# Kernel tuning notes

Hardware: AMD Instinct MI355X
Metric: run time of the kernel (lower is better)

The kernel has to match this reference:

```python
import jax, jax.numpy as jnp
import numpy as np

N = 100000
E = 400000
G = 2000  # number of graphs in batch
IN_DIM = 32
H = 192
L = 4
EPS = 1e-5


def setup_inputs() -> dict:
    key = jax.random.key(0)
    ks = jax.random.split(key, 20)
    x = jax.random.normal(ks[0], (N, IN_DIM), jnp.float32)
    edge_src = jax.random.randint(ks[1], (E,), 0, N, jnp.int32)
    edge_dst = jax.random.randint(ks[2], (E,), 0, N, jnp.int32)
    batch = jnp.sort(jax.random.randint(ks[3], (N,), 0, G, jnp.int32))
    s_in = 1.0 / np.sqrt(IN_DIM)
    s_h = 1.0 / np.sqrt(H)
    return {
        "x": x,
        "edge_src": edge_src,
        "edge_dst": edge_dst,
        "batch": batch,
        # layer 0 (in_dim -> H); weights stored [in, out]
        "Wrel0": jax.random.uniform(ks[4], (IN_DIM, H), jnp.float32, -s_in, s_in),
        "brel0": jax.random.uniform(ks[5], (H,), jnp.float32, -s_in, s_in),
        "Wroot0": jax.random.uniform(ks[6], (IN_DIM, H), jnp.float32, -s_in, s_in),
        # layers 1..3 stacked (H -> H)
        "Wrel": jax.random.uniform(ks[7], (L - 1, H, H), jnp.float32, -s_h, s_h),
        "brel": jax.random.uniform(ks[8], (L - 1, H), jnp.float32, -s_h, s_h),
        "Wroot": jax.random.uniform(ks[9], (L - 1, H, H), jnp.float32, -s_h, s_h),
        # batchnorm affine params for all 4 layers
        "gamma": jnp.ones((L, H), jnp.float32),
        "beta": jnp.zeros((L, H), jnp.float32),
        # head MLP and output
        "Wh1": jax.random.uniform(ks[10], (H, H), jnp.float32, -s_h, s_h),
        "bh1": jax.random.uniform(ks[11], (H,), jnp.float32, -s_h, s_h),
        "Wh2": jax.random.uniform(ks[12], (H, H), jnp.float32, -s_h, s_h),
        "bh2": jax.random.uniform(ks[13], (H,), jnp.float32, -s_h, s_h),
        "Wout": jax.random.uniform(ks[14], (H, 1), jnp.float32, -s_h, s_h),
        "bout": jax.random.uniform(ks[15], (1,), jnp.float32, -s_h, s_h),
    }


def _rel_conv(x, edge_src, edge_dst, Wrel, brel, Wroot):
    # message: lin_rel(x_j); applying the linear at node level first is the
    # same math as per-edge (linear commutes with gather) and cheaper.
    h = x @ Wrel + brel                      # [N, out]
    agg = jax.ops.segment_sum(h[edge_src], edge_dst, num_segments=N)
    return agg + x @ Wroot


def _bn_relu(h, g, b):
    # BatchNorm1d in training mode: batch stats over node dim, biased var
    mu = h.mean(axis=0)
    var = jnp.var(h, axis=0)
    h = (h - mu) * jax.lax.rsqrt(var + EPS) * g + b
    return jax.nn.relu(h)


def reference(x, edge_src, edge_dst, batch, Wrel0, brel0, Wroot0,
              Wrel, brel, Wroot, gamma, beta, Wh1, bh1, Wh2, bh2, Wout, bout):
    h = _bn_relu(_rel_conv(x, edge_src, edge_dst, Wrel0, brel0, Wroot0),
                 gamma[0], beta[0])
    for i in range(L - 1):
        h = _bn_relu(_rel_conv(h, edge_src, edge_dst, Wrel[i], brel[i], Wroot[i]),
                     gamma[i + 1], beta[i + 1])
    # global mean pool over graphs
    sums = jax.ops.segment_sum(h, batch, num_segments=G)          # [G, H]
    cnt = jax.ops.segment_sum(jnp.ones((N,), h.dtype), batch, num_segments=G)
    g = sums / jnp.maximum(cnt, 1.0)[:, None]
    # head MLP (dropout is identity at eval) + output linear
    g = jax.nn.relu(g @ Wh1 + bh1) @ Wh2 + bh2
    return g @ Wout + bout                                        # [G, 1]
```

## Files before the change

kernel.cpp:

```cpp
#include <hip/hip_runtime.h>

#define HDIM 192
#define EPS 1e-5f

typedef __attribute__((ext_vector_type(8))) _Float16 half8;
typedef __attribute__((ext_vector_type(4))) float floatx4;

__device__ __forceinline__ float h2f(ushort u) {
    union { ushort u; _Float16 h; } c; c.u = u; return (float)c.h;
}
__device__ __forceinline__ ushort f2h(float x) {
    _Float16 h = (_Float16)x;
    union { _Float16 h; ushort u; } c; c.h = h; return c.u;
}
__device__ __forceinline__ uint4 pack8(const ushort* h) {
    uint4 p;
    p.x = h[0] | ((uint)h[1] << 16); p.y = h[2] | ((uint)h[3] << 16);
    p.z = h[4] | ((uint)h[5] << 16); p.w = h[6] | ((uint)h[7] << 16);
    return p;
}

__device__ __forceinline__ void gload_lds16(const ushort* g, ushort* l) {
    __builtin_amdgcn_global_load_lds(
        (const __attribute__((address_space(1))) unsigned int*)g,
        (__attribute__((address_space(3))) unsigned int*)l, 16, 0, 0);
}

#define WAITV0() asm volatile("s_waitcnt vmcnt(0)" ::: "memory")


struct PrepArgs {
    const float* src[6];
    ushort*      dst[6];
    int K[6];
    int off[7];
};

__global__ __launch_bounds__(256) void prep_all_k(PrepArgs a)
{
    int idx = blockIdx.x * 256 + threadIdx.x;
    if (idx >= a.off[6]) return;
    int i = 0;
    #pragma unroll
    for (int t = 1; t < 6; ++t) if (idx >= a.off[t]) i = t;
    int r = idx - a.off[i];
    int K = a.K[i];
    int perMat = (K >> 5) * 12 * 64;
    int mat = r / perMat;
    r -= mat * perMat;
    int lane = r & 63;
    int ct = (r >> 6) % 12;
    int kc = r / (12 * 64);
    int col = ct * 16 + (lane & 15);
    int kb  = kc * 32 + (lane >> 4) * 8;
    const float* Wm = a.src[i] + (size_t)mat * K * HDIM;
    ushort* base = a.dst[i] + (size_t)mat * K * HDIM;
    size_t o = (size_t)kc * 6144 + (size_t)(ct * 64 + lane) * 8;
    #pragma unroll
    for (int j = 0; j < 8; ++j)
        base[o + j] = f2h(Wm[(size_t)(kb + j) * HDIM + col]);
}

__global__ __launch_bounds__(256) void conv_half_k(
    const float* __restrict__ src, ushort* __restrict__ dst, int R, int C)
{
    int OC = C >> 3;
    int idx = blockIdx.x * 256 + threadIdx.x;
    if (idx >= R * OC) return;
    int r = idx / OC;
    int o = idx - r * OC;
    float4 v0 = ((const float4*)(src + (size_t)r * C + o * 8))[0];
    float4 v1 = ((const float4*)(src + (size_t)r * C + o * 8))[1];
    float v[8] = {v0.x, v0.y, v0.z, v0.w, v1.x, v1.y, v1.z, v1.w};
    ushort h[8];
    #pragma unroll
    for (int t = 0; t < 8; ++t) h[t] = f2h(v[t]);
    *(uint4*)(dst + (size_t)r * C + o * 8) = pack8(h);
}

template<bool DUAL, bool RELU, bool DEG, bool STATS, int NKC>
__global__ __launch_bounds__(256, 3) void gemm_mfma_k(
    const ushort* __restrict__ A1h, const ushort* __restrict__ W1f,
    const ushort* __restrict__ A2h, const ushort* __restrict__ W2f,
    const float* __restrict__ degf, const float* __restrict__ bias,
    ushort* __restrict__ C, float* __restrict__ pstats, int N, int K)
{
    constexpr int KR   = NKC * 32;
    constexpr int RS   = KR + 8;
    constexpr int SLAB = 64 * RS;
    constexpr int NINSTR = SLAB / 512;
    constexpr int NCH  = DUAL ? 2 * NKC : NKC;
    constexpr int SMEMU = ((DUAL ? 2 * SLAB : SLAB) > 12800)
                            ? (DUAL ? 2 * SLAB : SLAB) : 12800;

    __shared__ float sstat[2][HDIM];
    __shared__ __align__(16) ushort smem[SMEMU];
    const int tid  = threadIdx.x;
    const int wave = tid >> 6;
    const int lane = tid & 63;
    const int row0 = blockIdx.x * 64;
    const int m16 = lane & 15;
    const int g4  = lane >> 4;

    if (STATS && tid < HDIM) { sstat[0][tid] = 0.f; sstat[1][tid] = 0.f; }

    auto stage = [&](const ushort* Ab, int slabOff) {
        #pragma unroll
        for (int i = wave; i < NINSTR; i += 4) {
            int slotB = i * 1024 + lane * 16;
            int r   = slotB / (RS * 2);
            int off = slotB - r * (RS * 2);
            if (off >= KR * 2) off = KR * 2 - 16;
            int rr = row0 + r; if (rr >= N) rr = N - 1;
            gload_lds16(Ab + (size_t)rr * KR + (off >> 1),
                        smem + slabOff + i * 512);
        }
    };

    stage(A1h, 0);
    if constexpr (DUAL) stage(A2h, SLAB);
    WAITV0();
    __builtin_amdgcn_s_barrier();
    __builtin_amdgcn_sched_barrier(0);

    auto loadB = [&](int c, half8* b) {
        bool ph = DUAL && (c >= NKC);
        int kc = ph ? c - NKC : c;
        const ushort* Bp = (ph ? W2f : W1f) + (size_t)kc * 6144
                         + (size_t)(wave * 192 + lane) * 8;
        #pragma unroll
        for (int ct = 0; ct < 3; ++ct)
            b[ct] = *(const half8*)(Bp + ct * 512);
    };

    floatx4 acc[4][3];
    #pragma unroll
    for (int s = 0; s < 4; ++s)
        #pragma unroll
        for (int ct = 0; ct < 3; ++ct) acc[s][ct] = (floatx4){0.f, 0.f, 0.f, 0.f};

    half8 bA[3], bB[3];
    loadB(0, bA);
    #pragma unroll
    for (int c = 0; c < NCH; ++c) {
        if (c + 1 < NCH) loadB(c + 1, (c & 1) ? bA : bB);
        const int base = (DUAL && c >= NKC) ? SLAB : 0;
        const int kc   = (DUAL && c >= NKC) ? c - NKC : c;
        const ushort* aB = smem + base + m16 * RS + kc * 32 + g4 * 8;
        half8 a[4];
        #pragma unroll
        for (int s = 0; s < 4; ++s)
            a[s] = *(const half8*)(aB + s * 16 * RS);
        const half8* bu = (c & 1) ? bB : bA;
        #pragma unroll
        for (int ct = 0; ct < 3; ++ct)
            #pragma unroll
            for (int s = 0; s < 4; ++s)
                acc[s][ct] = __builtin_amdgcn_mfma_f32_16x16x32_f16(a[s], bu[ct], acc[s][ct], 0, 0, 0);
    }

    __syncthreads();
    #pragma unroll
    for (int ct = 0; ct < 3; ++ct) {
        int col = wave * 48 + ct * 16 + m16;
        float bv = bias ? bias[col] : 0.f;
        float lsum = 0.f, lsq = 0.f;
        #pragma unroll
        for (int s = 0; s < 4; ++s) {
            #pragma unroll
            for (int reg = 0; reg < 4; ++reg) {
                int rloc = s * 16 + g4 * 4 + reg;
                int rr = row0 + rloc;
                int rrc = rr < N ? rr : N - 1;
                float v = acc[s][ct][reg] + (DEG ? degf[rrc] * bv : bv);
                if (STATS && rr < N) { lsum += v; lsq += v * v; }
                if (RELU) v = fmaxf(v, 0.f);
                smem[rloc * 200 + col] = f2h(v);
            }
        }
        if (STATS) {
            lsum += __shfl_xor(lsum, 16); lsum += __shfl_xor(lsum, 32);
            lsq  += __shfl_xor(lsq, 16);  lsq  += __shfl_xor(lsq, 32);
            if (g4 == 0) {
                atomicAdd(&sstat[0][col], lsum);
                atomicAdd(&sstat[1][col], lsq);
            }
        }
    }
    __syncthreads();
    {
        int rowsLeft = N - row0; if (rowsLeft > 64) rowsLeft = 64;
        int lim = rowsLeft * 24;
        ushort* Cb = C + (size_t)row0 * HDIM;
        #pragma unroll
        for (int k = 0; k < 6; ++k) {
            int u = tid + k * 256;
            if (u < lim) {
                int r  = u / 24;
                int c8 = (u - r * 24) * 8;
                *(uint4*)(Cb + (size_t)u * 8) =
                    *(const uint4*)(smem + r * 200 + c8);
            }
        }
    }
    if (STATS) {
        if (tid < HDIM) {
            float* pb = pstats + (size_t)blockIdx.x * (2 * HDIM);
            pb[tid]        = sstat[0][tid];
            pb[HDIM + tid] = sstat[1][tid];
        }
    }
}

__global__ __launch_bounds__(256) void bn_reduce_k(
    const float* __restrict__ pbuf, float* __restrict__ stats, int nb)
{
    __shared__ float red[32][9];
    int t  = threadIdx.x;
    int cl = t & 7;
    int s  = t >> 3;
    int c  = blockIdx.x * 8 + cl;
    float acc = 0.f;
    int b = s;
    for (; b + 96 < nb; b += 128) {
        float a0 = pbuf[(size_t)b * 384 + c];
        float a1 = pbuf[(size_t)(b + 32) * 384 + c];
        float a2 = pbuf[(size_t)(b + 64) * 384 + c];
        float a3 = pbuf[(size_t)(b + 96) * 384 + c];
        acc += a0 + a1 + a2 + a3;
    }
    for (; b < nb; b += 32)
        acc += pbuf[(size_t)b * 384 + c];
    red[s][cl] = acc;
    __syncthreads();
    if (t < 8) {
        float a = 0.f;
        #pragma unroll
        for (int i = 0; i < 32; ++i) a += red[i][t];
        stats[blockIdx.x * 8 + t] = a;
    }
}

__global__ __launch_bounds__(256) void hist_k(
    const int* __restrict__ dst, int* __restrict__ deg, int E)
{
    int e = blockIdx.x * 256 + threadIdx.x;
    if (e < E) atomicAdd(&deg[dst[e]], 1);
}

__global__ __launch_bounds__(256) void block_sum_k(
    const int* __restrict__ deg, int* __restrict__ bsum, int N)
{
    __shared__ int s[256];
    int t = threadIdx.x;
    int n = blockIdx.x * 256 + t;
    s[t] = (n < N) ? deg[n] : 0;
    __syncthreads();
    for (int off = 128; off > 0; off >>= 1) {
        if (t < off) s[t] += s[t + off];
        __syncthreads();
    }
    if (t == 0) bsum[blockIdx.x] = s[0];
}

__global__ __launch_bounds__(512) void scan_bsum_k(int* __restrict__ bsum, int nb)
{
    __shared__ int s[512];
    int t = threadIdx.x;
    int v = (t < nb) ? bsum[t] : 0;
    s[t] = v;
    __syncthreads();
    for (int off = 1; off < 512; off <<= 1) {
        int u = (t >= off) ? s[t - off] : 0;
        __syncthreads();
        s[t] += u;
        __syncthreads();
    }
    if (t < nb) bsum[t] = s[t] - v;
}

__global__ __launch_bounds__(256) void row_ptr_k(
    const int* __restrict__ deg, const int* __restrict__ bsum,
    int* __restrict__ row_ptr, int* __restrict__ cursor,
    float* __restrict__ degf, int N, int E)
{
    __shared__ int s[256];
    int t = threadIdx.x;
    int n = blockIdx.x * 256 + t;
    int v = (n < N) ? deg[n] : 0;
    s[t] = v;
    __syncthreads();
    for (int off = 1; off < 256; off <<= 1) {
        int u = (t >= off) ? s[t - off] : 0;
        __syncthreads();
        s[t] += u;
        __syncthreads();
    }
    int ex = s[t] - v + bsum[blockIdx.x];
    if (n < N) {
        row_ptr[n] = ex;
        cursor[n]  = ex;
        degf[n]    = (float)v;
    }
    if (blockIdx.x == 0 && t == 0) row_ptr[N] = E;
}

__global__ __launch_bounds__(256) void fill_k(
    const int* __restrict__ src, const int* __restrict__ dst,
    int* __restrict__ cursor, int* __restrict__ col, int E)
{
    int e = blockIdx.x * 256 + threadIdx.x;
    if (e < E) {
        int p = atomicAdd(&cursor[dst[e]], 1);
        col[p] = src[e];
    }
}

__global__ __launch_bounds__(256) void gather_h_k(
    const ushort* __restrict__ xh, const int* __restrict__ row_ptr,
    const int* __restrict__ col, ushort* __restrict__ gh, int N, int K)
{
    int OC = K >> 3;
    int idx = blockIdx.x * 256 + threadIdx.x;
    if (idx >= N * OC) return;
    int n = idx / OC;
    int o = idx - n * OC;
    const ushort* hp = xh + o * 8;
    int j0 = row_ptr[n], j1 = row_ptr[n + 1];
    float acc[8] = {0.f,0.f,0.f,0.f,0.f,0.f,0.f,0.f};
    auto addrow = [&](uint4 hv) {
        uint hu[4] = {hv.x, hv.y, hv.z, hv.w};
        #pragma unroll
        for (int t = 0; t < 4; ++t) {
            acc[2*t]   += h2f((ushort)(hu[t] & 0xffffu));
            acc[2*t+1] += h2f((ushort)(hu[t] >> 16));
        }
    };
    int j = j0;
    for (; j + 3 < j1; j += 4) {
        int s0 = col[j], s1 = col[j+1], s2 = col[j+2], s3 = col[j+3];
        uint4 v0 = *(const uint4*)(hp + (size_t)s0 * K);
        uint4 v1 = *(const uint4*)(hp + (size_t)s1 * K);
        uint4 v2 = *(const uint4*)(hp + (size_t)s2 * K);
        uint4 v3 = *(const uint4*)(hp + (size_t)s3 * K);
        addrow(v0); addrow(v1); addrow(v2); addrow(v3);
    }
    for (; j < j1; ++j)
        addrow(*(const uint4*)(hp + (size_t)col[j] * K));
    ushort oh[8];
    #pragma unroll
    for (int t = 0; t < 8; ++t) oh[t] = f2h(acc[t]);
    *(uint4*)(gh + (size_t)n * K + o * 8) = pack8(oh);
}

__global__ __launch_bounds__(256) void gather_bn_k(
    const ushort* __restrict__ h, const float* __restrict__ stats,
    const float* __restrict__ gamma, const float* __restrict__ beta,
    float invN, const int* __restrict__ row_ptr, const int* __restrict__ col,
    ushort* __restrict__ xh, ushort* __restrict__ gh, int N)
{
    int idx = blockIdx.x * 256 + threadIdx.x;
    if (idx >= N * 24) return;
    int n = idx / 24;
    int o = idx - n * 24;
    int q = o * 8;
    float sc[8], sh[8];
    #pragma unroll
    for (int t = 0; t < 8; ++t) {
        float mu  = stats[q + t] * invN;
        float var = stats[HDIM + q + t] * invN - mu * mu;
        float s = gamma[q + t] * rsqrtf(var + EPS);
        sc[t] = s; sh[t] = beta[q + t] - mu * s;
    }
    const ushort* hp = h + q;
    {
        uint4 hv = *(const uint4*)(hp + (size_t)n * HDIM);
        uint hu[4] = {hv.x, hv.y, hv.z, hv.w};
        ushort oh[8];
        #pragma unroll
        for (int t = 0; t < 4; ++t) {
            float v0 = h2f((ushort)(hu[t] & 0xffffu));
            float v1 = h2f((ushort)(hu[t] >> 16));
            oh[2*t]   = f2h(fmaxf(v0 * sc[2*t]   + sh[2*t],   0.f));
            oh[2*t+1] = f2h(fmaxf(v1 * sc[2*t+1] + sh[2*t+1], 0.f));
        }
        *(uint4*)(xh + (size_t)n * HDIM + q) = pack8(oh);
    }
    int j0 = row_ptr[n], j1 = row_ptr[n + 1];
    float acc[8] = {0.f,0.f,0.f,0.f,0.f,0.f,0.f,0.f};
    auto addrow = [&](uint4 hv) {
        uint hu[4] = {hv.x, hv.y, hv.z, hv.w};
        #pragma unroll
        for (int t = 0; t < 4; ++t) {
            float v0 = h2f((ushort)(hu[t] & 0xffffu));
            float v1 = h2f((ushort)(hu[t] >> 16));
            acc[2*t]   += fmaxf(v0 * sc[2*t]   + sh[2*t],   0.f);
            acc[2*t+1] += fmaxf(v1 * sc[2*t+1] + sh[2*t+1], 0.f);
        }
    };
    int j = j0;
    for (; j + 3 < j1; j += 4) {
        int s0 = col[j], s1 = col[j+1], s2 = col[j+2], s3 = col[j+3];
        uint4 v0 = *(const uint4*)(hp + (size_t)s0 * HDIM);
        uint4 v1 = *(const uint4*)(hp + (size_t)s1 * HDIM);
        uint4 v2 = *(const uint4*)(hp + (size_t)s2 * HDIM);
        uint4 v3 = *(const uint4*)(hp + (size_t)s3 * HDIM);
        addrow(v0); addrow(v1); addrow(v2); addrow(v3);
    }
    for (; j < j1; ++j)
        addrow(*(const uint4*)(hp + (size_t)col[j] * HDIM));
    ushort oh[8];
    #pragma unroll
    for (int t = 0; t < 8; ++t) oh[t] = f2h(acc[t]);
    *(uint4*)(gh + (size_t)n * HDIM + q) = pack8(oh);
}

__global__ __launch_bounds__(192) void pool_bn_k(
    const ushort* __restrict__ h, const float* __restrict__ stats,
    const float* __restrict__ gamma, const float* __restrict__ beta,
    float invN, const int* __restrict__ batch,
    ushort* __restrict__ gsh, int G, int N)
{
    __shared__ int bounds[2];
    int g = blockIdx.x;
    int c = threadIdx.x;
    if (c < 2) {
        int key = g + c;
        int lo = 0, hi = N;
        while (lo < hi) {
            int mid = (lo + hi) >> 1;
            if (batch[mid] < key) lo = mid + 1; else hi = mid;
        }
        bounds[c] = lo;
    }
    __syncthreads();
    int r0 = bounds[0], r1 = bounds[1];
    float mu  = stats[c] * invN;
    float var = stats[HDIM + c] * invN - mu * mu;
    float sc  = gamma[c] * rsqrtf(var + EPS);
    float sh  = beta[c] - mu * sc;
    const ushort* base = h + c;
    float s = 0.f;
    for (int r = r0; r < r1; ++r)
        s += fmaxf(h2f(base[(size_t)r * HDIM]) * sc + sh, 0.f);
    float m = s / fmaxf((float)(r1 - r0), 1.f);
    gsh[(size_t)g * HDIM + c] = f2h(m);
}

__global__ __launch_bounds__(64) void out_dot_k(
    const ushort* __restrict__ g2h, const float* __restrict__ Wout,
    const float* __restrict__ bout, float* __restrict__ out, int G)
{
    int gi = blockIdx.x;
    int t = threadIdx.x;
    float s = 0.f;
    #pragma unroll
    for (int j = 0; j < 3; ++j) {
        int c = t + j * 64;
        s += h2f(g2h[(size_t)gi * HDIM + c]) * Wout[c];
    }
    #pragma unroll
    for (int off = 32; off > 0; off >>= 1) s += __shfl_down(s, off, 64);
    if (t == 0) out[gi] = s + bout[0];
}

extern "C" void kernel_launch(void* const* d_in, const int* in_sizes, int n_in,
                              void* d_out, int out_size, void* d_ws, size_t ws_size,
                              hipStream_t stream)
{
    const float* x      = (const float*)d_in[0];
    const int*   esrc   = (const int*)d_in[1];
    const int*   edst   = (const int*)d_in[2];
    const int*   batch  = (const int*)d_in[3];
    const float* Wrel0  = (const float*)d_in[4];
    const float* brel0  = (const float*)d_in[5];
    const float* Wroot0 = (const float*)d_in[6];
    const float* Wrel   = (const float*)d_in[7];
    const float* brel   = (const float*)d_in[8];
    const float* Wroot  = (const float*)d_in[9];
    const float* gamma  = (const float*)d_in[10];
    const float* beta   = (const float*)d_in[11];
    const float* Wh1    = (const float*)d_in[12];
    const float* bh1    = (const float*)d_in[13];
    const float* Wh2    = (const float*)d_in[14];
    const float* bh2    = (const float*)d_in[15];
    const float* Wout   = (const float*)d_in[16];
    const float* bout   = (const float*)d_in[17];
    float* out = (float*)d_out;

    const int N  = in_sizes[3];
    const int E  = in_sizes[1];
    const int K0 = in_sizes[0] / N;
    const int G  = out_size;
    const int nBlocks = (N + 255) / 256;
    const float invN = 1.0f / (float)N;

    char* p = (char*)d_ws;
    auto carve = [&](size_t bytes) -> void* {
        void* r = (void*)p; p += (bytes + 255) & ~(size_t)255; return r;
    };
    ushort* bufa_h= (ushort*)carve((size_t)N * HDIM * 2);
    ushort* xh    = (ushort*)carve((size_t)N * HDIM * 2);
    ushort* gh    = (ushort*)carve((size_t)N * HDIM * 2);
    ushort* gsh   = (ushort*)carve((size_t)G * HDIM * 2);
    ushort* g1h   = (ushort*)carve((size_t)G * HDIM * 2);
    ushort* g2h   = (ushort*)carve((size_t)G * HDIM * 2);
    int*    deg   = (int*)   carve((size_t)N * 4);
    float*  bnsums= (float*) carve(4 * 2 * HDIM * 4);
    size_t  zspan = (char*)(bnsums + 4 * 2 * HDIM) - (char*)deg;
    float*  degf  = (float*) carve((size_t)N * 4);
    int*    row_ptr=(int*)   carve((size_t)(N + 1) * 4);
    int*    cursor= (int*)   carve((size_t)N * 4);
    int*    col   = (int*)   carve((size_t)E * 4);
    int*    bsum  = (int*)   carve((size_t)nBlocks * 4);
    ushort* Wrel0f= (ushort*)carve((size_t)K0 * HDIM * 2);
    ushort* Wroot0f=(ushort*)carve((size_t)K0 * HDIM * 2);
    ushort* Wrelf = (ushort*)carve((size_t)3 * HDIM * HDIM * 2);
    ushort* Wrootf= (ushort*)carve((size_t)3 * HDIM * HDIM * 2);
    ushort* Wh1f  = (ushort*)carve((size_t)HDIM * HDIM * 2);
    ushort* Wh2f  = (ushort*)carve((size_t)HDIM * HDIM * 2);

    dim3 b256(256);
    const int eBlocks = (E + 255) / 256;
    const int gemmN = (N + 63) / 64;
    const int gemmG = (G + 63) / 64;

    float*  pbuf  = (float*) carve((size_t)gemmN * 2 * HDIM * 4);

    {
        PrepArgs a;
        int t0 = (K0 >> 5) * 12 * 64;
        int t1 = (HDIM >> 5) * 12 * 64;
        a.src[0] = Wrel0;  a.dst[0] = Wrel0f;  a.K[0] = K0;
        a.src[1] = Wroot0; a.dst[1] = Wroot0f; a.K[1] = K0;
        a.src[2] = Wrel;   a.dst[2] = Wrelf;   a.K[2] = HDIM;
        a.src[3] = Wroot;  a.dst[3] = Wrootf;  a.K[3] = HDIM;
        a.src[4] = Wh1;    a.dst[4] = Wh1f;    a.K[4] = HDIM;
        a.src[5] = Wh2;    a.dst[5] = Wh2f;    a.K[5] = HDIM;
        a.off[0] = 0;
        a.off[1] = a.off[0] + t0;
        a.off[2] = a.off[1] + t0;
        a.off[3] = a.off[2] + 3 * t1;
        a.off[4] = a.off[3] + 3 * t1;
        a.off[5] = a.off[4] + t1;
        a.off[6] = a.off[5] + t1;
        prep_all_k<<<(a.off[6] + 255) / 256, b256, 0, stream>>>(a);
    }
    conv_half_k<<<((N * (K0 >> 3)) + 255) / 256, b256, 0, stream>>>(x, xh, N, K0);

    hipMemsetAsync(deg, 0, zspan, stream);
    hist_k<<<eBlocks, b256, 0, stream>>>(edst, deg, E);
    block_sum_k<<<nBlocks, b256, 0, stream>>>(deg, bsum, N);
    scan_bsum_k<<<1, dim3(512), 0, stream>>>(bsum, nBlocks);
    row_ptr_k<<<nBlocks, b256, 0, stream>>>(deg, bsum, row_ptr, cursor, degf, N, E);
    fill_k<<<eBlocks, b256, 0, stream>>>(esrc, edst, cursor, col, E);

    gather_h_k<<<((N * (K0 >> 3)) + 255) / 256, b256, 0, stream>>>(
        xh, row_ptr, col, gh, N, K0);
    gemm_mfma_k<true, false, true, true, 1><<<gemmN, b256, 0, stream>>>(
        gh, Wrel0f, xh, Wroot0f, degf, brel0, bufa_h, pbuf, N, K0);
    bn_reduce_k<<<48, b256, 0, stream>>>(pbuf, bnsums, gemmN);

    for (int l = 1; l < 4; ++l) {
        const ushort* Wrf = Wrelf  + (size_t)(l - 1) * HDIM * HDIM;
        const ushort* Wtf = Wrootf + (size_t)(l - 1) * HDIM * HDIM;
        const float*  br  = brel   + (size_t)(l - 1) * HDIM;
        gather_bn_k<<<(N * 24 + 255) / 256, b256, 0, stream>>>(
            bufa_h, bnsums + (l - 1) * 2 * HDIM,
            gamma + (l - 1) * HDIM, beta + (l - 1) * HDIM, invN,
            row_ptr, col, xh, gh, N);
        gemm_mfma_k<true, false, true, true, 6><<<gemmN, b256, 0, stream>>>(
            gh, Wrf, xh, Wtf, degf, br, bufa_h, pbuf, N, HDIM);
        bn_reduce_k<<<48, b256, 0, stream>>>(pbuf, bnsums + l * 2 * HDIM, gemmN);
    }

    pool_bn_k<<<G, dim3(192), 0, stream>>>(
        bufa_h, bnsums + 3 * 2 * HDIM, gamma + 3 * HDIM, beta + 3 * HDIM,
        invN, batch, gsh, G, N);

    gemm_mfma_k<false, true, false, false, 6><<<gemmG, b256, 0, stream>>>(
        gsh, Wh1f, nullptr, nullptr, nullptr, bh1, g1h, nullptr, G, HDIM);
    gemm_mfma_k<false, false, false, false, 6><<<gemmG, b256, 0, stream>>>(
        g1h, Wh2f, nullptr, nullptr, nullptr, bh2, g2h, nullptr, G, HDIM);
    out_dot_k<<<G, dim3(64), 0, stream>>>(g2h, Wout, bout, out, G);
}
```

Baseline: 474.1 us.

## Fuse BatchNorm+ReLU of the root operand into the GEMM LDS stage

The gather kernel no longer writes a normalized copy (xh) of the previous layer's activations. Instead, the dual GEMM stages the raw previous-layer half activations into LDS and applies BatchNorm scale/shift plus ReLU in place in shared memory before the MFMA loop. This removes one full N×192 half-precision write per layer and its later re-read. In exchange it adds an LDS pass and extra barriers inside the GEMM, and the GEMM now reads and writes the same buffer in place, relying on each block owning its rows.

After: 456.1 us. -3.8%, faster.

```diff
diff --git a/kernel.cpp b/kernel.cpp
--- a/kernel.cpp
+++ b/kernel.cpp
@@ -78,11 +78,13 @@
     *(uint4*)(dst + (size_t)r * C + o * 8) = pack8(h);
 }
 
-template<bool DUAL, bool RELU, bool DEG, bool STATS, int NKC>
+template<bool DUAL, bool RELU, bool DEG, bool STATS, bool BNIN, int NKC>
 __global__ __launch_bounds__(256, 3) void gemm_mfma_k(
     const ushort* __restrict__ A1h, const ushort* __restrict__ W1f,
     const ushort* __restrict__ A2h, const ushort* __restrict__ W2f,
     const float* __restrict__ degf, const float* __restrict__ bias,
+    const float* __restrict__ instats, const float* __restrict__ gammaL,
+    const float* __restrict__ betaL, float invN,
     ushort* __restrict__ C, float* __restrict__ pstats, int N, int K)
 {
     constexpr int KR   = NKC * 32;
@@ -102,7 +104,7 @@
     const int m16 = lane & 15;
     const int g4  = lane >> 4;
 
-    if (STATS && tid < HDIM) { sstat[0][tid] = 0.f; sstat[1][tid] = 0.f; }
+    if (STATS && !BNIN && tid < HDIM) { sstat[0][tid] = 0.f; sstat[1][tid] = 0.f; }
 
     auto stage = [&](const ushort* Ab, int slabOff) {
         #pragma unroll
@@ -122,6 +124,38 @@
     WAITV0();
     __builtin_amdgcn_s_barrier();
     __builtin_amdgcn_sched_barrier(0);
+
+    if constexpr (BNIN) {
+        if (tid < HDIM) {
+            float mu  = instats[tid] * invN;
+            float var = instats[HDIM + tid] * invN - mu * mu;
+            float s = gammaL[tid] * rsqrtf(var + EPS);
+            sstat[0][tid] = s;
+            sstat[1][tid] = betaL[tid] - mu * s;
+        }
+        __syncthreads();
+        {
+            int r = tid >> 2, q = tid & 3;
+            ushort* rowp = smem + SLAB + r * RS + q * 48;
+            #pragma unroll
+            for (int k = 0; k < 6; ++k) {
+                uint4 hv = *(uint4*)(rowp + k * 8);
+                uint hu[4] = {hv.x, hv.y, hv.z, hv.w};
+                ushort oh[8];
+                #pragma unroll
+                for (int e = 0; e < 4; ++e) {
+                    int ch = q * 48 + k * 8 + e * 2;
+                    float v0 = h2f((ushort)(hu[e] & 0xffffu)) * sstat[0][ch]     + sstat[1][ch];
+                    float v1 = h2f((ushort)(hu[e] >> 16))     * sstat[0][ch + 1] + sstat[1][ch + 1];
+                    oh[2*e]   = f2h(fmaxf(v0, 0.f));
+                    oh[2*e+1] = f2h(fmaxf(v1, 0.f));
+                }
+                *(uint4*)(rowp + k * 8) = pack8(oh);
+            }
+        }
+        __syncthreads();
+        if (STATS && tid < HDIM) { sstat[0][tid] = 0.f; sstat[1][tid] = 0.f; }
+    }
 
     auto loadB = [&](int c, half8* b) {
         bool ph = DUAL && (c >= NKC);
@@ -357,7 +391,7 @@
     const ushort* __restrict__ h, const float* __restrict__ stats,
     const float* __restrict__ gamma, const float* __restrict__ beta,
     float invN, const int* __restrict__ row_ptr, const int* __restrict__ col,
-    ushort* __restrict__ xh, ushort* __restrict__ gh, int N)
+    ushort* __restrict__ gh, int N)
 {
     int idx = blockIdx.x * 256 + threadIdx.x;
     if (idx >= N * 24) return;
@@ -373,19 +407,6 @@
         sc[t] = s; sh[t] = beta[q + t] - mu * s;
     }
     const ushort* hp = h + q;
-    {
-        uint4 hv = *(const uint4*)(hp + (size_t)n * HDIM);
-        uint hu[4] = {hv.x, hv.y, hv.z, hv.w};
-        ushort oh[8];
-        #pragma unroll
-        for (int t = 0; t < 4; ++t) {
-            float v0 = h2f((ushort)(hu[t] & 0xffffu));
-            float v1 = h2f((ushort)(hu[t] >> 16));
-            oh[2*t]   = f2h(fmaxf(v0 * sc[2*t]   + sh[2*t],   0.f));
-            oh[2*t+1] = f2h(fmaxf(v1 * sc[2*t+1] + sh[2*t+1], 0.f));
-        }
-        *(uint4*)(xh + (size_t)n * HDIM + q) = pack8(oh);
-    }
     int j0 = row_ptr[n], j1 = row_ptr[n + 1];
     float acc[8] = {0.f,0.f,0.f,0.f,0.f,0.f,0.f,0.f};
     auto addrow = [&](uint4 hv) {
@@ -557,20 +578,23 @@
 
     gather_h_k<<<((N * (K0 >> 3)) + 255) / 256, b256, 0, stream>>>(
         xh, row_ptr, col, gh, N, K0);
-    gemm_mfma_k<true, false, true, true, 1><<<gemmN, b256, 0, stream>>>(
-        gh, Wrel0f, xh, Wroot0f, degf, brel0, bufa_h, pbuf, N, K0);
+    gemm_mfma_k<true, false, true, true, false, 1><<<gemmN, b256, 0, stream>>>(
+        gh, Wrel0f, xh, Wroot0f, degf, brel0,
+        nullptr, nullptr, nullptr, 0.f, bufa_h, pbuf, N, K0);
     bn_reduce_k<<<48, b256, 0, stream>>>(pbuf, bnsums, gemmN);
 
     for (int l = 1; l < 4; ++l) {
         const ushort* Wrf = Wrelf  + (size_t)(l - 1) * HDIM * HDIM;
         const ushort* Wtf = Wrootf + (size_t)(l - 1) * HDIM * HDIM;
         const float*  br  = brel   + (size_t)(l - 1) * HDIM;
+        const float*  st  = bnsums + (size_t)(l - 1) * 2 * HDIM;
+        const float*  gm  = gamma  + (size_t)(l - 1) * HDIM;
+        const float*  bt  = beta   + (size_t)(l - 1) * HDIM;
         gather_bn_k<<<(N * 24 + 255) / 256, b256, 0, stream>>>(
-            bufa_h, bnsums + (l - 1) * 2 * HDIM,
-            gamma + (l - 1) * HDIM, beta + (l - 1) * HDIM, invN,
-            row_ptr, col, xh, gh, N);
-        gemm_mfma_k<true, false, true, true, 6><<<gemmN, b256, 0, stream>>>(
-            gh, Wrf, xh, Wtf, degf, br, bufa_h, pbuf, N, HDIM);
+            bufa_h, st, gm, bt, invN, row_ptr, col, gh, N);
+        gemm_mfma_k<true, false, true, true, true, 6><<<gemmN, b256, 0, stream>>>(
+            gh, Wrf, bufa_h, Wtf, degf, br,
+            st, gm, bt, invN, bufa_h, pbuf, N, HDIM);
         bn_reduce_k<<<48, b256, 0, stream>>>(pbuf, bnsums + l * 2 * HDIM, gemmN);
     }
 
@@ -578,9 +602,11 @@
         bufa_h, bnsums + 3 * 2 * HDIM, gamma + 3 * HDIM, beta + 3 * HDIM,
         invN, batch, gsh, G, N);
 
-    gemm_mfma_k<false, true, false, false, 6><<<gemmG, b256, 0, stream>>>(
-        gsh, Wh1f, nullptr, nullptr, nullptr, bh1, g1h, nullptr, G, HDIM);
-    gemm_mfma_k<false, false, false, false, 6><<<gemmG, b256, 0, stream>>>(
-        g1h, Wh2f, nullptr, nullptr, nullptr, bh2, g2h, nullptr, G, HDIM);
+    gemm_mfma_k<false, true, false, false, false, 6><<<gemmG, b256, 0, stream>>>(
+        gsh, Wh1f, nullptr, nullptr, nullptr, bh1,
+        nullptr, nullptr, nullptr, 0.f, g1h, nullptr, G, HDIM);
+    gemm_mfma_k<false, false, false, false, false, 6><<<gemmG, b256, 0, stream>>>(
+        g1h, Wh2f, nullptr, nullptr, nullptr, bh2,
+        nullptr, nullptr, nullptr, 0.f, g2h, nullptr, G, HDIM);
     out_dot_k<<<G, dim3(64), 0, stream>>>(g2h, Wout, bout, out, G);
 }
```
